# Performance work log

Measured on AMD Instinct MI355X. Metric: run time of the kernel, lower is better.

Reference implementation:

```python
import jax, jax.numpy as jnp
import numpy as np

TOTAL_REL = 500
EMB_DIM = 256
TOTAL_ENT = 400000
BATCH = 2048


def setup_inputs() -> dict:
    key = jax.random.key(0)
    k1, k2, k3, k4, k5 = jax.random.split(key, 5)
    batch_h = jax.random.randint(k1, (BATCH,), 0, TOTAL_ENT, dtype=jnp.int64 if jax.config.jax_enable_x64 else jnp.int32)
    batch_t = jax.random.randint(k2, (BATCH,), 0, TOTAL_ENT, dtype=batch_h.dtype)
    batch_r = jax.random.randint(k3, (BATCH,), 0, TOTAL_REL, dtype=batch_h.dtype)
    ent_emb = jax.random.normal(k4, (TOTAL_ENT, EMB_DIM), dtype=jnp.float32)
    # Parameter: rel_emb = diag_embed(rand(R, d)) -> (R, d, d) with random diagonal
    rel_vec = jax.random.uniform(k5, (TOTAL_REL, EMB_DIM), dtype=jnp.float32)
    rel_emb = rel_vec[:, :, None] * jnp.eye(EMB_DIM, dtype=jnp.float32)  # (R, d, d)
    return {"batch_h": batch_h, "batch_t": batch_t, "batch_r": batch_r,
            "ent_emb": ent_emb, "rel_emb": rel_emb}


def reference(batch_h, batch_t, batch_r, ent_emb, rel_emb):
    heads = ent_emb[batch_h]            # (B, d)
    tails = ent_emb[batch_t]            # (B, d)
    rels = rel_emb[batch_r]             # (B, d, d) per-example relation matrix
    # heads_i @ rels_i  -> (B, d); then all-pairs against tails.T -> (B, B)
    hr = jnp.einsum('bd,bde->be', heads, rels)
    score = jax.nn.sigmoid(jnp.einsum('be,ce->bc', hr, tails))
    return score
```

## Files before the change

### kernel.cpp

```cpp
#include <hip/hip_runtime.h>
#include <hip/hip_fp16.h>

#define TOTAL_RELN 500
#define EMB 256
#define NBATCH 2048
#define KSPLIT 768

typedef _Float16 half8 __attribute__((ext_vector_type(8)));
typedef float f32x4 __attribute__((ext_vector_type(4)));

__device__ __forceinline__ void gload_lds16(const void* g, void* l) {
    __builtin_amdgcn_global_load_lds(
        (const __attribute__((address_space(1))) void*)g,
        (__attribute__((address_space(3))) void*)l, 16, 0, 0);
}

__global__ __launch_bounds__(EMB) void prep_kernel(
    const int* __restrict__ bh, const int* __restrict__ bt,
    const int* __restrict__ br, const float* __restrict__ ent,
    const float* __restrict__ rel, _Float16* __restrict__ Ap,
    _Float16* __restrict__ Bp) {
    const int b = blockIdx.x;
    const int e = threadIdx.x;
    const int h = bh[b], t = bt[b], r = br[b];

    const float hv = ent[(size_t)h * EMB + e];
    const float rv = rel[(size_t)r * EMB * EMB + (size_t)e * (EMB + 1)];
    const float tv = ent[(size_t)t * EMB + e];
    const float hr = hv * rv;

    const _Float16 a_hi = (_Float16)hr;
    const _Float16 a_lo = (_Float16)(hr - (float)a_hi);
    const _Float16 b_hi = (_Float16)tv;
    const _Float16 b_lo = (_Float16)(tv - (float)b_hi);

    const size_t base = (size_t)b * KSPLIT;
    Ap[base + e]           = a_hi;
    Ap[base + EMB + e]     = a_lo;
    Ap[base + 2 * EMB + e] = a_hi;
    Bp[base + e]           = b_hi;
    Bp[base + EMB + e]     = b_hi;
    Bp[base + 2 * EMB + e] = b_lo;
}

#define BM 128
#define BN 128
#define BK 64

__global__ __launch_bounds__(256) void gemm_sig_kernel(
    const _Float16* __restrict__ Ap, const _Float16* __restrict__ Bp,
    float* __restrict__ out) {
    __shared__ _Float16 As[BM * BK];
    __shared__ _Float16 Bs[BN * BK];

    const int tid  = threadIdx.x;
    const int wave = tid >> 6;
    const int lane = tid & 63;
    const int bm = blockIdx.y, bn = blockIdx.x;
    const int wr = wave >> 1, wc = wave & 1;

    f32x4 acc[4][4] = {};

    const int l8  = lane >> 3;
    const int c16 = (lane & 7) * 16;

    for (int kt = 0; kt < KSPLIT / BK; ++kt) {
        __syncthreads();
        const int k0 = kt * BK;
        #pragma unroll
        for (int rnd = 0; rnd < 4; ++rnd) {
            const int rowbase = rnd * 32 + wave * 8;
            const char* ga = (const char*)(Ap + (size_t)(bm * BM + rowbase + l8) * KSPLIT + k0) + c16;
            gload_lds16(ga, (char*)As + rowbase * (BK * 2));
            const char* gb = (const char*)(Bp + (size_t)(bn * BN + rowbase + l8) * KSPLIT + k0) + c16;
            gload_lds16(gb, (char*)Bs + rowbase * (BK * 2));
        }
        __syncthreads();

        #pragma unroll
        for (int ks = 0; ks < 2; ++ks) {
            half8 af[4], bf[4];
            const int kb = ks * 32 + (lane >> 4) * 8;
            const int rA = lane & 15;
            #pragma unroll
            for (int m = 0; m < 4; ++m)
                af[m] = *(const half8*)&As[(wr * 64 + m * 16 + rA) * BK + kb];
            #pragma unroll
            for (int n = 0; n < 4; ++n)
                bf[n] = *(const half8*)&Bs[(wc * 64 + n * 16 + rA) * BK + kb];
            #pragma unroll
            for (int m = 0; m < 4; ++m)
                #pragma unroll
                for (int n = 0; n < 4; ++n)
                    acc[m][n] = __builtin_amdgcn_mfma_f32_16x16x32_f16(
                        af[m], bf[n], acc[m][n], 0, 0, 0);
        }
    }

    const int row0 = bm * BM + wr * 64;
    const int col0 = bn * BN + wc * 64;
    const int rlane = (lane >> 4) * 4;
    const int clane = lane & 15;
    #pragma unroll
    for (int m = 0; m < 4; ++m)
        #pragma unroll
        for (int n = 0; n < 4; ++n)
            #pragma unroll
            for (int j = 0; j < 4; ++j) {
                const float v = acc[m][n][j];
                const float s = 1.0f / (1.0f + expf(-v));
                out[(size_t)(row0 + m * 16 + rlane + j) * NBATCH
                    + (col0 + n * 16 + clane)] = s;
            }
}

extern "C" void kernel_launch(void* const* d_in, const int* in_sizes, int n_in,
                              void* d_out, int out_size, void* d_ws, size_t ws_size,
                              hipStream_t stream) {
    const int*   batch_h = (const int*)d_in[0];
    const int*   batch_t = (const int*)d_in[1];
    const int*   batch_r = (const int*)d_in[2];
    const float* ent_emb = (const float*)d_in[3];
    const float* rel_emb = (const float*)d_in[4];
    float* out = (float*)d_out;

    _Float16* Ap = (_Float16*)d_ws;
    _Float16* Bp = Ap + (size_t)NBATCH * KSPLIT;

    prep_kernel<<<NBATCH, EMB, 0, stream>>>(batch_h, batch_t, batch_r,
                                            ent_emb, rel_emb, Ap, Bp);
    gemm_sig_kernel<<<dim3(NBATCH / BN, NBATCH / BM), 256, 0, stream>>>(Ap, Bp, out);
}
```

Before: 524.1 us.

## Double-buffer GEMM LDS tiles, use 8 waves per block, swizzle block order

The GEMM kernel now double-buffers the A/B tiles in LDS, issuing the next tile's global-to-LDS loads before computing the current one, so memory latency overlaps with MFMA work. The block grows to 512 threads (8 waves, each computing a 32x64 sub-tile), and a 1D grid with a block-index swizzle changes tile ordering for better L2 reuse. The sigmoid switches to the fast __expf intrinsic. This doubles LDS use and halves per-wave accumulators. There is a possible race: the next stage's async loads are issued before the current compute without waiting on the outstanding loads (vmcnt), relying on __syncthreads only.

```diff
diff --git a/kernel.cpp b/kernel.cpp
--- a/kernel.cpp
+++ b/kernel.cpp
@@ -46,71 +46,89 @@
 #define BM 128
 #define BN 128
 #define BK 64
+#define KTILES (KSPLIT / BK)
 
-__global__ __launch_bounds__(256) void gemm_sig_kernel(
+__global__ __launch_bounds__(512) void gemm_sig_kernel(
     const _Float16* __restrict__ Ap, const _Float16* __restrict__ Bp,
     float* __restrict__ out) {
-    __shared__ _Float16 As[BM * BK];
-    __shared__ _Float16 Bs[BN * BK];
+    __shared__ _Float16 As[2][BM * BK];
+    __shared__ _Float16 Bs[2][BN * BK];
 
     const int tid  = threadIdx.x;
     const int wave = tid >> 6;
     const int lane = tid & 63;
-    const int bm = blockIdx.y, bn = blockIdx.x;
-    const int wr = wave >> 1, wc = wave & 1;
 
-    f32x4 acc[4][4] = {};
+    const int bid = blockIdx.x;
+    const int swz = (bid & 7) * 32 + (bid >> 3);
+    const int bm = swz >> 4, bn = swz & 15;
+
+    const int wr = wave >> 1;
+    const int wc = wave & 1;
+
+    f32x4 acc[2][4] = {};
 
     const int l8  = lane >> 3;
     const int c16 = (lane & 7) * 16;
 
-    for (int kt = 0; kt < KSPLIT / BK; ++kt) {
-        __syncthreads();
+    const _Float16* Abase = Ap + (size_t)(bm * BM) * KSPLIT;
+    const _Float16* Bbase = Bp + (size_t)(bn * BN) * KSPLIT;
+
+    auto stage = [&](int buf, int kt) {
         const int k0 = kt * BK;
         #pragma unroll
-        for (int rnd = 0; rnd < 4; ++rnd) {
-            const int rowbase = rnd * 32 + wave * 8;
-            const char* ga = (const char*)(Ap + (size_t)(bm * BM + rowbase + l8) * KSPLIT + k0) + c16;
-            gload_lds16(ga, (char*)As + rowbase * (BK * 2));
-            const char* gb = (const char*)(Bp + (size_t)(bn * BN + rowbase + l8) * KSPLIT + k0) + c16;
-            gload_lds16(gb, (char*)Bs + rowbase * (BK * 2));
+        for (int rnd = 0; rnd < 2; ++rnd) {
+            const int rowbase = rnd * 64 + wave * 8;
+            gload_lds16(
+                (const char*)(Abase + (size_t)(rowbase + l8) * KSPLIT + k0) + c16,
+                (char*)&As[buf][rowbase * BK]);
+            gload_lds16(
+                (const char*)(Bbase + (size_t)(rowbase + l8) * KSPLIT + k0) + c16,
+                (char*)&Bs[buf][rowbase * BK]);
         }
-        __syncthreads();
+    };
 
+    auto compute = [&](int buf) {
         #pragma unroll
         for (int ks = 0; ks < 2; ++ks) {
-            half8 af[4], bf[4];
-            const int kb = ks * 32 + (lane >> 4) * 8;
+            const int kb = ks * 32 + ((lane >> 4) << 3);
             const int rA = lane & 15;
+            half8 af[2], bf[4];
             #pragma unroll
-            for (int m = 0; m < 4; ++m)
-                af[m] = *(const half8*)&As[(wr * 64 + m * 16 + rA) * BK + kb];
+            for (int m = 0; m < 2; ++m)
+                af[m] = *(const half8*)&As[buf][(wr * 32 + m * 16 + rA) * BK + kb];
             #pragma unroll
             for (int n = 0; n < 4; ++n)
-                bf[n] = *(const half8*)&Bs[(wc * 64 + n * 16 + rA) * BK + kb];
+                bf[n] = *(const half8*)&Bs[buf][(wc * 64 + n * 16 + rA) * BK + kb];
             #pragma unroll
-            for (int m = 0; m < 4; ++m)
+            for (int m = 0; m < 2; ++m)
                 #pragma unroll
                 for (int n = 0; n < 4; ++n)
                     acc[m][n] = __builtin_amdgcn_mfma_f32_16x16x32_f16(
                         af[m], bf[n], acc[m][n], 0, 0, 0);
         }
+    };
+
+    stage(0, 0);
+    __syncthreads();
+    int buf = 0;
+    for (int kt = 0; kt < KTILES; ++kt) {
+        if (kt + 1 < KTILES) stage(buf ^ 1, kt + 1);
+        compute(buf);
+        __syncthreads();
+        buf ^= 1;
     }
 
-    const int row0 = bm * BM + wr * 64;
-    const int col0 = bn * BN + wc * 64;
-    const int rlane = (lane >> 4) * 4;
-    const int clane = lane & 15;
+    const int row0 = bm * BM + wr * 32 + ((lane >> 4) << 2);
+    const int col0 = bn * BN + wc * 64 + (lane & 15);
     #pragma unroll
-    for (int m = 0; m < 4; ++m)
+    for (int m = 0; m < 2; ++m)
         #pragma unroll
         for (int n = 0; n < 4; ++n)
             #pragma unroll
             for (int j = 0; j < 4; ++j) {
                 const float v = acc[m][n][j];
-                const float s = 1.0f / (1.0f + expf(-v));
-                out[(size_t)(row0 + m * 16 + rlane + j) * NBATCH
-                    + (col0 + n * 16 + clane)] = s;
+                const float s = 1.0f / (1.0f + __expf(-v));
+                out[(size_t)(row0 + m * 16 + j) * NBATCH + (col0 + n * 16)] = s;
             }
 }
 
@@ -129,5 +147,5 @@
 
     prep_kernel<<<NBATCH, EMB, 0, stream>>>(batch_h, batch_t, batch_r,
                                             ent_emb, rel_emb, Ap, Bp);
-    gemm_sig_kernel<<<dim3(NBATCH / BN, NBATCH / BM), 256, 0, stream>>>(Ap, Bp, out);
+    gemm_sig_kernel<<<256, 512, 0, stream>>>(Ap, Bp, out);
 }
```

Measured after the change: 520.5 us. About the same (-0.7%).
